# Optimization experiments

Hardware: AMD Instinct MI355X
Metric: run time of the kernel (lower is better)

The kernel has to match this reference:

```python
import jax, jax.numpy as jnp
import numpy as np

B, D, L = 16384, 2048, 6

def setup_inputs() -> dict:
    key = jax.random.key(0)
    kx, kw = jax.random.split(key)
    x = jax.random.normal(kx, (B, D), dtype=jnp.float32)
    # cross weights: xavier_normal on (D,1) -> std = sqrt(2/(D+1)); stacked [L, D]
    std = float(np.sqrt(2.0 / (D + 1)))
    W = jax.random.normal(kw, (L, D), dtype=jnp.float32) * std
    b = jnp.zeros((L, D), dtype=jnp.float32)  # bias params init to zeros
    return {"x": x, "W": W, "b": b}

def reference(x, W, b):
    # Original per layer: x_l = (x0 @ x_l^T) @ w_i + b_i + x_l
    # Algebraically identical: x_l = x0 * (x_l . w_i) + b_i + x_l  (scalar per row)
    x_l = x
    for i in range(W.shape[0]):
        s = jnp.einsum('bd,d->b', x_l, W[i])          # [B]
        x_l = x * s[:, None] + b[i][None, :] + x_l     # [B, D]
    return x_l
```

## Files before the change

### kernel.cpp

```cpp
#include <hip/hip_runtime.h>

#define B_ROWS   16384
#define D_DIM    2048
#define L_LAYERS 6

#define THREADS  512
#define WPB      (THREADS / 64)
#define ROWS_PER_WAVE 4
#define TOTAL_WAVES (B_ROWS / ROWS_PER_WAVE)
#define BLOCKS   (TOTAL_WAVES / WPB)
#define PRE_THREADS 1024
#define WS_FLOATS   (D_DIM + L_LAYERS)

typedef float f32x4 __attribute__((ext_vector_type(4)));


__global__ __launch_bounds__(PRE_THREADS) void precompute_Ue(
    const float* __restrict__ W,
    const float* __restrict__ b,
    float* __restrict__ ws)
{
    __shared__ float red[PRE_THREADS / 64][L_LAYERS];
    const int t    = threadIdx.x;
    const int lane = t & 63;
    const int wid  = t >> 6;
    const int base = t * 2;

    float2 prefix = make_float2(0.f, 0.f);
    float e_red[L_LAYERS];
    #pragma unroll
    for (int l = 0; l < L_LAYERS; ++l) {
        const float2 wv = *(const float2*)(W + l * D_DIM + base);
        const float2 bv = *(const float2*)(b + l * D_DIM + base);
        e_red[l] = prefix.x * wv.x + prefix.y * wv.y;
        prefix.x += bv.x; prefix.y += bv.y;
    }
    *(float2*)(ws + base) = prefix;
    #pragma unroll
    for (int l = 0; l < L_LAYERS; ++l) {
        float v = e_red[l];
        #pragma unroll
        for (int off = 32; off >= 1; off >>= 1) v += __shfl_xor(v, off, 64);
        if (lane == 0) red[wid][l] = v;
    }
    __syncthreads();
    if (t < L_LAYERS) {
        float s = 0.f;
        #pragma unroll
        for (int w = 0; w < PRE_THREADS / 64; ++w) s += red[w][t];
        ws[D_DIM + t] = s;
    }
}

template <bool USE_WS>
__global__ __launch_bounds__(THREADS) void cross_rows(
    const float* __restrict__ x,
    const float* __restrict__ W,
    const float* __restrict__ b,
    const float* __restrict__ ws,
    float* __restrict__ out)
{
    __shared__ float Wl[L_LAYERS][D_DIM];
    __shared__ float Ul[D_DIM];
    __shared__ float eLs[L_LAYERS];
    __shared__ float red[WPB][L_LAYERS];

    const int t    = threadIdx.x;
    const int lane = t & 63;
    const int wid  = t >> 6;
    const int sbase = t * 4;

    #pragma unroll
    for (int l = 0; l < L_LAYERS; ++l)
        *(float4*)&Wl[l][sbase] = *(const float4*)(W + l * D_DIM + sbase);
    if constexpr (USE_WS) {
        *(float4*)&Ul[sbase] = *(const float4*)(ws + sbase);
        if (t < L_LAYERS) eLs[t] = ws[D_DIM + t];
    } else {
        float4 prefix = make_float4(0.f, 0.f, 0.f, 0.f);
        float e_red[L_LAYERS];
        #pragma unroll
        for (int l = 0; l < L_LAYERS; ++l) {
            const float4 wv = *(const float4*)(W + l * D_DIM + sbase);
            const float4 bv = *(const float4*)(b + l * D_DIM + sbase);
            e_red[l] = prefix.x * wv.x + prefix.y * wv.y
                     + prefix.z * wv.z + prefix.w * wv.w;
            prefix.x += bv.x; prefix.y += bv.y;
            prefix.z += bv.z; prefix.w += bv.w;
        }
        *(float4*)&Ul[sbase] = prefix;
        #pragma unroll
        for (int l = 0; l < L_LAYERS; ++l) {
            float v = e_red[l];
            #pragma unroll
            for (int off = 32; off >= 1; off >>= 1) v += __shfl_xor(v, off, 64);
            if (lane == 0) red[wid][l] = v;
        }
        __syncthreads();
        if (t < L_LAYERS) {
            float s = 0.f;
            #pragma unroll
            for (int w = 0; w < WPB; ++w) s += red[w][t];
            eLs[t] = s;
        }
    }
    __syncthreads();

    const int gw = blockIdx.x * WPB + wid;
    const float* xr = x + (size_t)gw * ROWS_PER_WAVE * D_DIM;
    float* orow     = out + (size_t)gw * ROWS_PER_WAVE * D_DIM;
    const int eoff  = lane * 4;

    float p[ROWS_PER_WAVE][L_LAYERS];
    #pragma unroll
    for (int r = 0; r < ROWS_PER_WAVE; ++r)
        #pragma unroll
        for (int l = 0; l < L_LAYERS; ++l) p[r][l] = 0.f;

    #pragma unroll 2
    for (int j = 0; j < 8; ++j) {
        float4 wv[L_LAYERS];
        #pragma unroll
        for (int l = 0; l < L_LAYERS; ++l)
            wv[l] = *(const float4*)&Wl[l][j * 256 + eoff];
        #pragma unroll
        for (int r = 0; r < ROWS_PER_WAVE; ++r) {
            const float4 xv = *(const float4*)(xr + (size_t)r * D_DIM + j * 256 + eoff);
            #pragma unroll
            for (int l = 0; l < L_LAYERS; ++l)
                p[r][l] += xv.x * wv[l].x + xv.y * wv[l].y
                         + xv.z * wv[l].z + xv.w * wv[l].w;
        }
    }

    #pragma unroll
    for (int off = 32; off >= 1; off >>= 1) {
        #pragma unroll
        for (int r = 0; r < ROWS_PER_WAVE; ++r)
            #pragma unroll
            for (int l = 0; l < L_LAYERS; ++l)
                p[r][l] += __shfl_xor(p[r][l], off, 64);
    }

    float c[ROWS_PER_WAVE];
    #pragma unroll
    for (int r = 0; r < ROWS_PER_WAVE; ++r) {
        float cr = 1.f;
        #pragma unroll
        for (int l = 0; l < L_LAYERS; ++l)
            cr = cr * (1.f + p[r][l]) + eLs[l];
        c[r] = cr;
    }

    #pragma unroll 2
    for (int j = 0; j < 8; ++j) {
        const float4 uv = *(const float4*)&Ul[j * 256 + eoff];
        #pragma unroll
        for (int r = 0; r < ROWS_PER_WAVE; ++r) {
            const size_t off = (size_t)r * D_DIM + j * 256 + eoff;
            const float4 xv = *(const float4*)(xr + off);
            f32x4 o;
            o.x = c[r] * xv.x + uv.x; o.y = c[r] * xv.y + uv.y;
            o.z = c[r] * xv.z + uv.z; o.w = c[r] * xv.w + uv.w;
            __builtin_nontemporal_store(o, (f32x4*)(orow + off));
        }
    }
}

extern "C" void kernel_launch(void* const* d_in, const int* in_sizes, int n_in,
                              void* d_out, int out_size, void* d_ws, size_t ws_size,
                              hipStream_t stream) {
    (void)in_sizes; (void)n_in; (void)out_size;
    const float* x = (const float*)d_in[0];
    const float* W = (const float*)d_in[1];
    const float* b = (const float*)d_in[2];
    float* out = (float*)d_out;

    const bool use_ws = (d_ws != nullptr) && (ws_size >= WS_FLOATS * sizeof(float));
    if (use_ws) {
        float* ws = (float*)d_ws;
        precompute_Ue<<<dim3(1), dim3(PRE_THREADS), 0, stream>>>(W, b, ws);
        cross_rows<true><<<dim3(BLOCKS), dim3(THREADS), 0, stream>>>(
            x, W, b, ws, out);
    } else {
        cross_rows<false><<<dim3(BLOCKS), dim3(THREADS), 0, stream>>>(
            x, W, b, nullptr, out);
    }
}
```

Baseline: 251.7 us.

## Split fused cross kernel into separate dot pass and streaming apply pass

Replaces the single fused row kernel with two kernels. The first computes per-row dot products with the layer weights and writes one scalar coefficient per row to workspace. The second is a flat grid-stride streaming kernel that computes c*x+U. This simplifies the apply pass and removes the weight staging in shared memory, but x must be read twice from global memory and an extra launch is added. The workspace requirement grows, and a fallback fused kernel runs when it is too small.

```diff
diff --git a/kernel.cpp b/kernel.cpp
--- a/kernel.cpp
+++ b/kernel.cpp
@@ -4,13 +4,23 @@
 #define D_DIM    2048
 #define L_LAYERS 6
 
-#define THREADS  512
-#define WPB      (THREADS / 64)
-#define ROWS_PER_WAVE 4
-#define TOTAL_WAVES (B_ROWS / ROWS_PER_WAVE)
-#define BLOCKS   (TOTAL_WAVES / WPB)
 #define PRE_THREADS 1024
-#define WS_FLOATS   (D_DIM + L_LAYERS)
+
+#define WS_U_OFF   0
+#define WS_E_OFF   D_DIM
+#define WS_C_OFF   (D_DIM + 16)
+#define WS_FLOATS  (WS_C_OFF + B_ROWS)
+
+#define P1_THREADS 256
+#define P1_WAVES   (P1_THREADS / 64)
+#define P1_ROWS_PER_WAVE 2
+#define P1_BLOCKS  (B_ROWS / (P1_WAVES * P1_ROWS_PER_WAVE))
+
+#define P2_THREADS 256
+#define P2_BLOCKS  4096
+#define P2_TOTAL_F4 (B_ROWS * (D_DIM / 4))
+#define P2_STRIDE   (P2_BLOCKS * P2_THREADS)
+#define P2_ITERS    (P2_TOTAL_F4 / P2_STRIDE)
 
 typedef float f32x4 __attribute__((ext_vector_type(4)));
 
@@ -35,7 +45,7 @@
         e_red[l] = prefix.x * wv.x + prefix.y * wv.y;
         prefix.x += bv.x; prefix.y += bv.y;
     }
-    *(float2*)(ws + base) = prefix;
+    *(float2*)(ws + WS_U_OFF + base) = prefix;
     #pragma unroll
     for (int l = 0; l < L_LAYERS; ++l) {
         float v = e_red[l];
@@ -48,35 +58,109 @@
         float s = 0.f;
         #pragma unroll
         for (int w = 0; w < PRE_THREADS / 64; ++w) s += red[w][t];
-        ws[D_DIM + t] = s;
-    }
-}
-
-template <bool USE_WS>
-__global__ __launch_bounds__(THREADS) void cross_rows(
+        ws[WS_E_OFF + t] = s;
+    }
+}
+
+__global__ __launch_bounds__(P1_THREADS) void pass1_dots(
+    const float* __restrict__ x,
+    const float* __restrict__ W,
+    const float* __restrict__ ws_in,
+    float* __restrict__ ws_c)
+{
+    const int t    = threadIdx.x;
+    const int lane = t & 63;
+    const int wid  = t >> 6;
+    const int gw   = blockIdx.x * P1_WAVES + wid;
+    const size_t r0 = (size_t)gw * P1_ROWS_PER_WAVE;
+    const float* xr0 = x + r0 * D_DIM;
+    const float* xr1 = xr0 + D_DIM;
+    const int eoff = lane * 4;
+
+    float p0[L_LAYERS], p1[L_LAYERS];
+    #pragma unroll
+    for (int l = 0; l < L_LAYERS; ++l) { p0[l] = 0.f; p1[l] = 0.f; }
+
+    #pragma unroll 2
+    for (int j = 0; j < 8; ++j) {
+        const float4 xv0 = *(const float4*)(xr0 + j * 256 + eoff);
+        const float4 xv1 = *(const float4*)(xr1 + j * 256 + eoff);
+        #pragma unroll
+        for (int l = 0; l < L_LAYERS; ++l) {
+            const float4 wv = *(const float4*)(W + l * D_DIM + j * 256 + eoff);
+            p0[l] += xv0.x * wv.x + xv0.y * wv.y + xv0.z * wv.z + xv0.w * wv.w;
+            p1[l] += xv1.x * wv.x + xv1.y * wv.y + xv1.z * wv.z + xv1.w * wv.w;
+        }
+    }
+
+    #pragma unroll
+    for (int off = 32; off >= 1; off >>= 1) {
+        #pragma unroll
+        for (int l = 0; l < L_LAYERS; ++l) {
+            p0[l] += __shfl_xor(p0[l], off, 64);
+            p1[l] += __shfl_xor(p1[l], off, 64);
+        }
+    }
+
+    float c0 = 1.f, c1 = 1.f;
+    #pragma unroll
+    for (int l = 0; l < L_LAYERS; ++l) {
+        const float el = ws_in[WS_E_OFF + l];
+        c0 = c0 * (1.f + p0[l]) + el;
+        c1 = c1 * (1.f + p1[l]) + el;
+    }
+    if (lane == 0) {
+        ws_c[r0]     = c0;
+        ws_c[r0 + 1] = c1;
+    }
+}
+
+__global__ __launch_bounds__(P2_THREADS) void pass2_apply(
+    const float* __restrict__ x,
+    const float* __restrict__ ws,
+    float* __restrict__ out)
+{
+    const f32x4* x4 = (const f32x4*)x;
+    const f32x4* U4 = (const f32x4*)(ws + WS_U_OFF);
+    const float* cv = ws + WS_C_OFF;
+    f32x4* o4 = (f32x4*)out;
+
+    const int tid = blockIdx.x * P2_THREADS + threadIdx.x;
+    #pragma unroll 2
+    for (int k = 0; k < P2_ITERS; ++k) {
+        const int i   = tid + k * P2_STRIDE;
+        const int row = i >> 9;
+        const int d4  = i & 511;
+        const float c = cv[row];
+        const f32x4 xv = x4[i];
+        const f32x4 uv = U4[d4];
+        const f32x4 o = c * xv + uv;
+        __builtin_nontemporal_store(o, &o4[i]);
+    }
+}
+
+#define FB_THREADS 512
+#define FB_WPB     (FB_THREADS / 64)
+#define FB_ROWS_PER_WAVE 4
+#define FB_BLOCKS  (B_ROWS / (FB_ROWS_PER_WAVE * FB_WPB))
+
+__global__ __launch_bounds__(FB_THREADS) void cross_rows_fb(
     const float* __restrict__ x,
     const float* __restrict__ W,
     const float* __restrict__ b,
-    const float* __restrict__ ws,
     float* __restrict__ out)
 {
     __shared__ float Wl[L_LAYERS][D_DIM];
     __shared__ float Ul[D_DIM];
     __shared__ float eLs[L_LAYERS];
-    __shared__ float red[WPB][L_LAYERS];
+    __shared__ float red[FB_WPB][L_LAYERS];
 
     const int t    = threadIdx.x;
     const int lane = t & 63;
     const int wid  = t >> 6;
     const int sbase = t * 4;
 
-    #pragma unroll
-    for (int l = 0; l < L_LAYERS; ++l)
-        *(float4*)&Wl[l][sbase] = *(const float4*)(W + l * D_DIM + sbase);
-    if constexpr (USE_WS) {
-        *(float4*)&Ul[sbase] = *(const float4*)(ws + sbase);
-        if (t < L_LAYERS) eLs[t] = ws[D_DIM + t];
-    } else {
+    {
         float4 prefix = make_float4(0.f, 0.f, 0.f, 0.f);
         float e_red[L_LAYERS];
         #pragma unroll
@@ -87,6 +171,7 @@
                      + prefix.z * wv.z + prefix.w * wv.w;
             prefix.x += bv.x; prefix.y += bv.y;
             prefix.z += bv.z; prefix.w += bv.w;
+            *(float4*)&Wl[l][sbase] = wv;
         }
         *(float4*)&Ul[sbase] = prefix;
         #pragma unroll
@@ -100,20 +185,20 @@
         if (t < L_LAYERS) {
             float s = 0.f;
             #pragma unroll
-            for (int w = 0; w < WPB; ++w) s += red[w][t];
+            for (int w = 0; w < FB_WPB; ++w) s += red[w][t];
             eLs[t] = s;
         }
     }
     __syncthreads();
 
-    const int gw = blockIdx.x * WPB + wid;
-    const float* xr = x + (size_t)gw * ROWS_PER_WAVE * D_DIM;
-    float* orow     = out + (size_t)gw * ROWS_PER_WAVE * D_DIM;
+    const int gw = blockIdx.x * FB_WPB + wid;
+    const float* xr = x + (size_t)gw * FB_ROWS_PER_WAVE * D_DIM;
+    float* orow     = out + (size_t)gw * FB_ROWS_PER_WAVE * D_DIM;
     const int eoff  = lane * 4;
 
-    float p[ROWS_PER_WAVE][L_LAYERS];
-    #pragma unroll
-    for (int r = 0; r < ROWS_PER_WAVE; ++r)
+    float p[FB_ROWS_PER_WAVE][L_LAYERS];
+    #pragma unroll
+    for (int r = 0; r < FB_ROWS_PER_WAVE; ++r)
         #pragma unroll
         for (int l = 0; l < L_LAYERS; ++l) p[r][l] = 0.f;
 
@@ -124,7 +209,7 @@
         for (int l = 0; l < L_LAYERS; ++l)
             wv[l] = *(const float4*)&Wl[l][j * 256 + eoff];
         #pragma unroll
-        for (int r = 0; r < ROWS_PER_WAVE; ++r) {
+        for (int r = 0; r < FB_ROWS_PER_WAVE; ++r) {
             const float4 xv = *(const float4*)(xr + (size_t)r * D_DIM + j * 256 + eoff);
             #pragma unroll
             for (int l = 0; l < L_LAYERS; ++l)
@@ -136,15 +221,15 @@
     #pragma unroll
     for (int off = 32; off >= 1; off >>= 1) {
         #pragma unroll
-        for (int r = 0; r < ROWS_PER_WAVE; ++r)
+        for (int r = 0; r < FB_ROWS_PER_WAVE; ++r)
             #pragma unroll
             for (int l = 0; l < L_LAYERS; ++l)
                 p[r][l] += __shfl_xor(p[r][l], off, 64);
     }
 
-    float c[ROWS_PER_WAVE];
-    #pragma unroll
-    for (int r = 0; r < ROWS_PER_WAVE; ++r) {
+    float c[FB_ROWS_PER_WAVE];
+    #pragma unroll
+    for (int r = 0; r < FB_ROWS_PER_WAVE; ++r) {
         float cr = 1.f;
         #pragma unroll
         for (int l = 0; l < L_LAYERS; ++l)
@@ -156,13 +241,13 @@
     for (int j = 0; j < 8; ++j) {
         const float4 uv = *(const float4*)&Ul[j * 256 + eoff];
         #pragma unroll
-        for (int r = 0; r < ROWS_PER_WAVE; ++r) {
-            const size_t off = (size_t)r * D_DIM + j * 256 + eoff;
-            const float4 xv = *(const float4*)(xr + off);
+        for (int r = 0; r < FB_ROWS_PER_WAVE; ++r) {
+            const size_t off2 = (size_t)r * D_DIM + j * 256 + eoff;
+            const float4 xv = *(const float4*)(xr + off2);
             f32x4 o;
             o.x = c[r] * xv.x + uv.x; o.y = c[r] * xv.y + uv.y;
             o.z = c[r] * xv.z + uv.z; o.w = c[r] * xv.w + uv.w;
-            __builtin_nontemporal_store(o, (f32x4*)(orow + off));
+            __builtin_nontemporal_store(o, (f32x4*)(orow + off2));
         }
     }
 }
@@ -180,10 +265,12 @@
     if (use_ws) {
         float* ws = (float*)d_ws;
         precompute_Ue<<<dim3(1), dim3(PRE_THREADS), 0, stream>>>(W, b, ws);
-        cross_rows<true><<<dim3(BLOCKS), dim3(THREADS), 0, stream>>>(
-            x, W, b, ws, out);
+        pass1_dots<<<dim3(P1_BLOCKS), dim3(P1_THREADS), 0, stream>>>(
+            x, W, ws, ws + WS_C_OFF);
+        pass2_apply<<<dim3(P2_BLOCKS), dim3(P2_THREADS), 0, stream>>>(
+            x, ws, out);
     } else {
-        cross_rows<false><<<dim3(BLOCKS), dim3(THREADS), 0, stream>>>(
-            x, W, b, nullptr, out);
-    }
-}
+        cross_rows_fb<<<dim3(FB_BLOCKS), dim3(FB_THREADS), 0, stream>>>(
+            x, W, b, out);
+    }
+}
```

Result: slower. 265.0 us (+5.3%).
